# Performance work log

Measured on AMD Instinct MI355X. Metric: run time of the kernel, lower is better.

The kernel has to match this reference:

```python
import jax, jax.numpy as jnp
import numpy as np

B, T, S, E = 32, 256, 16, 400   # batch, max seq len, words per news, embed_size
H = 400                          # args.hidden_size (BiLSTM output width)
HC = H // 2                      # per-direction LSTM hidden
NH = 20                          # MHA heads (embed_size % 20 == 0)
DH = E // NH

def _p(k, shape, scale=0.05):
    return jax.random.normal(k, shape, dtype=jnp.float32) * scale

def setup_inputs():
    ks = jax.random.split(jax.random.key(0), 16)
    z = lambda n: jnp.zeros((n,), jnp.float32)
    return {
        "x1": jax.random.normal(ks[0], (B, T, E), dtype=jnp.float32),
        "x2": jax.random.normal(ks[1], (B, T, S, E), dtype=jnp.float32),
        "cate": jax.random.normal(ks[2], (B, T, 20), dtype=jnp.float32),
        "seq_lens": jnp.sort(jax.random.randint(ks[3], (B,), T // 2, T + 1))[::-1],
        "w_ih_f": _p(ks[4], (4 * HC, E)), "w_hh_f": _p(ks[5], (4 * HC, HC)),
        "b_ih_f": z(4 * HC), "b_hh_f": z(4 * HC),
        "w_ih_b": _p(ks[6], (4 * HC, E)), "w_hh_b": _p(ks[7], (4 * HC, HC)),
        "b_ih_b": z(4 * HC), "b_hh_b": z(4 * HC),
        "w_q": _p(ks[8], (E, E)), "b_q": z(E),
        "w_k": _p(ks[9], (E, E)), "b_k": z(E),
        "w_mlp_mha": _p(ks[10], (H, E)), "b_mlp_mha": z(H),
        "W_attn": _p(ks[11], (2 * H, 1)), "b_attn": z(1),
        "w_mlp": _p(ks[12], (E, 2 * H)), "b_mlp": z(E),
    }

def _lstm(x_tbe, w_ih, w_hh, b_ih, b_hh):
    # x_tbe: [T, B, in] -> [T, B, HC]; PyTorch gate order i,f,g,o
    h0 = jnp.zeros((x_tbe.shape[1], w_hh.shape[1]), x_tbe.dtype)
    def step(carry, xt):
        h, c = carry
        g = xt @ w_ih.T + h @ w_hh.T + (b_ih + b_hh)
        i, f, gg, o = jnp.split(g, 4, axis=-1)
        c = jax.nn.sigmoid(f) * c + jax.nn.sigmoid(i) * jnp.tanh(gg)
        h = jax.nn.sigmoid(o) * jnp.tanh(c)
        return (h, c), h
    _, hs = jax.lax.scan(step, (h0, h0), x_tbe)
    return hs

def reference(x1, x2, cate, seq_lens, w_ih_f, w_hh_f, b_ih_f, b_hh_f,
              w_ih_b, w_hh_b, b_ih_b, b_hh_b, w_q, b_q, w_k, b_k,
              w_mlp_mha, b_mlp_mha, W_attn, b_attn, w_mlp, b_mlp):
    t_idx = jnp.arange(T)
    valid = t_idx[None, :] < seq_lens[:, None]             # [B,T] ragged mask

    # --- per-news word self-attention pooling (only MHA attn weights used) ---
    tok = x2.reshape(B * T, S, E)
    q = (tok @ w_q.T + b_q).reshape(-1, S, NH, DH)
    k = (tok @ w_k.T + b_k).reshape(-1, S, NH, DH)
    scores = jnp.einsum('nqhd,nkhd->nhqk', q, k) * (1.0 / DH ** 0.5)
    w = jax.nn.softmax(scores, axis=-1).mean(axis=1)       # head-averaged [N,S,S]
    w = jax.nn.softmax(w.mean(axis=2), axis=1)             # [N,S]
    pooled = jnp.einsum('ns,nse->ne', w, tok)              # [N,E]
    x2p = (pooled @ w_mlp_mha.T + b_mlp_mha).reshape(B, T, H)

    # --- BiLSTM, equivalent to packed-sequence processing (per-length reversal) ---
    h_fwd = _lstm(x1.transpose(1, 0, 2), w_ih_f, w_hh_f, b_ih_f, b_hh_f).transpose(1, 0, 2)
    rev = jnp.clip(seq_lens[:, None] - 1 - t_idx[None, :], 0, T - 1)   # involution per seq
    x1r = jnp.take_along_axis(x1, rev[:, :, None], axis=1)
    h_bwd_r = _lstm(x1r.transpose(1, 0, 2), w_ih_b, w_hh_b, b_ih_b, b_hh_b).transpose(1, 0, 2)
    h_bwd = jnp.take_along_axis(h_bwd_r, rev[:, :, None], axis=1)
    h = jnp.concatenate([h_fwd, h_bwd], axis=-1)           # [B,T,H]

    # --- growing-window (causal) attention: score[b,t,s] = [h_s; x2p_t]@W_attn + b ---
    a = (h @ W_attn[:H]).squeeze(-1)                       # key term   [B,T]
    c = (x2p @ W_attn[H:]).squeeze(-1) + b_attn[0]         # query term [B,T]
    logits = a[:, None, :] + c[:, :, None]                 # [B,Tq,Tk]
    causal = t_idx[:, None] >= t_idx[None, :]
    attn = jax.nn.softmax(jnp.where(causal[None], logits, -1e30), axis=-1)
    x1_att = jnp.einsum('bts,bsh->bth', attn, h)           # [B,T,H]
    out = jnp.concatenate([x1_att, x2p], axis=-1) @ w_mlp.T + b_mlp
    return out * valid[:, :, None]                         # zeros beyond seq_lens
```

## Files before the change

kernel.cpp:

```cpp
#include <hip/hip_runtime.h>
#include <hip/hip_bf16.h>
#include <cstdint>
#include <cstddef>

typedef unsigned short u16;
typedef __attribute__((ext_vector_type(8))) short short8v;
typedef __attribute__((ext_vector_type(4))) short short4v;
typedef __attribute__((ext_vector_type(4))) float f32x4;
typedef __attribute__((ext_vector_type(4))) int i32x4;

#define MFMA16 __builtin_amdgcn_mfma_f32_16x16x32_bf16
#define MFMAI8 __builtin_amdgcn_mfma_i32_16x16x64_i8

__device__ __forceinline__ float bf2f(u16 u){
  union { unsigned int i; float f; } v; v.i = ((unsigned int)u) << 16; return v.f;
}
__device__ __forceinline__ u16 f2bf(float f){
  union { float f; unsigned int u; } v; v.f = f;
  unsigned int r = v.u + 0x7FFFu + ((v.u >> 16) & 1u);
  return (u16)(r >> 16);
}
__device__ __forceinline__ short8v szero(){
  short8v z;
  #pragma unroll
  for (int i = 0; i < 8; i++) z[i] = 0;
  return z;
}
__device__ __forceinline__ float sigm(float x){ return 1.0f/(1.0f + __expf(-x)); }
__device__ __forceinline__ float tanh_u(float x){
  float e = __expf(2.f*x);
  return 1.f - 2.f/(e + 1.f);
}
__device__ __forceinline__ void lds_barrier(){
  asm volatile("s_waitcnt lgkmcnt(0)" ::: "memory");
  __builtin_amdgcn_s_barrier();
  __builtin_amdgcn_sched_barrier(0);
}

__global__ void k0_cvt(const float* __restrict__ wq, const float* __restrict__ wk,
                       const float* __restrict__ wihf, const float* __restrict__ wihb,
                       const float* __restrict__ bihf, const float* __restrict__ bhhf,
                       const float* __restrict__ bihb, const float* __restrict__ bhhb,
                       u16* __restrict__ wqb, u16* __restrict__ wkb,
                       u16* __restrict__ wihfb, u16* __restrict__ wihbb,
                       float* __restrict__ bgf, float* __restrict__ bgb){
  int i = blockIdx.x*256 + threadIdx.x;
  if (i < 160000){ wqb[i] = f2bf(wq[i]); wkb[i] = f2bf(wk[i]); }
  if (i < 320000){ wihfb[i] = f2bf(wihf[i]); wihbb[i] = f2bf(wihb[i]); }
  if (i < 800){ bgf[i] = bihf[i] + bhhf[i]; bgb[i] = bihb[i] + bhhb[i]; }
}

__global__ void k0b_quant(const float* __restrict__ whhf, const float* __restrict__ whhb,
                          signed char* __restrict__ w8f, signed char* __restrict__ w8b,
                          float* __restrict__ sclf, float* __restrict__ sclb){
  const int tid = threadIdx.x, lane = tid & 63, wv = tid >> 6;
  const int widx = blockIdx.x*4 + wv;
  if (widx < 1600){
    int dir = widx / 800, g = widx - dir*800;
    const float* src = (dir ? whhb : whhf) + (size_t)g*200;
    float mx = 0.f;
    for (int j = lane; j < 200; j += 64) mx = fmaxf(mx, fabsf(src[j]));
    #pragma unroll
    for (int m = 32; m > 0; m >>= 1) mx = fmaxf(mx, __shfl_xor(mx, m, 64));
    float inv = (mx > 0.f) ? 127.f/mx : 0.f;
    int gt = g / 200, hl = g - gt*200;
    signed char* dst = (dir ? w8b : w8f) + (size_t)(gt*208 + hl)*256;
    int e0 = lane*4;
    unsigned int pack = 0u;
    if (e0 < 200){
      #pragma unroll
      for (int r = 0; r < 4; r++){
        int qv = __float2int_rn(src[e0+r]*inv);
        pack |= ((unsigned int)(qv & 255)) << (8*r);
      }
    }
    ((unsigned int*)dst)[lane] = pack;
    if (lane == 0) (dir ? sclb : sclf)[g] = mx / 16129.f;
  } else {
    int pr = widx - 1600;
    int dir = pr >> 5, rem = pr & 31, gt = rem >> 3, hl = 200 + (rem & 7);
    signed char* dst = (dir ? w8b : w8f) + (size_t)(gt*208 + hl)*256;
    ((unsigned int*)dst)[lane] = 0u;
  }
}

__launch_bounds__(512)
__global__ void k3_xw(const float* __restrict__ x1, const int* __restrict__ seq,
                      const u16* __restrict__ wihfb, const u16* __restrict__ wihbb,
                      const float* __restrict__ bgf, const float* __restrict__ bgb,
                      u16* __restrict__ xWf, u16* __restrict__ xWb){
  __shared__ u16 xf[12800];
  __shared__ u16 xb[12800];
  const int tid = threadIdx.x;
  const int t = blockIdx.x;
  for (int i = tid; i < 3200; i += 512){
    int b = i / 100, e4 = i - b*100;
    f32x4 vf = *(const f32x4*)&x1[((size_t)b*256 + t)*400 + e4*4];
    int rb = seq[b] - 1 - t; if (rb < 0) rb = 0;
    f32x4 vb = *(const f32x4*)&x1[((size_t)b*256 + rb)*400 + e4*4];
    short4v sf, sb;
    #pragma unroll
    for (int r = 0; r < 4; r++){ sf[r] = f2bf(vf[r]); sb[r] = f2bf(vb[r]); }
    ((short4v*)xf)[i] = sf;
    ((short4v*)xb)[i] = sb;
  }
  __syncthreads();
  const int lane = tid & 63, wv = tid >> 6;
  const int dir = wv >> 2, wl = wv & 3;
  const u16* xs = dir ? xb : xf;
  const u16* W  = dir ? wihbb : wihfb;
  const float* bg = dir ? bgb : bgf;
  u16* xW = dir ? xWb : xWf;
  const int q = lane & 15, kg = lane >> 4;
  short8v A[2][13];
  #pragma unroll
  for (int mt = 0; mt < 2; mt++)
    #pragma unroll
    for (int ksi = 0; ksi < 13; ksi++){
      int e0 = ksi*32 + kg*8;
      A[mt][ksi] = (e0 < 400) ? *(const short8v*)&xs[(mt*16 + q)*400 + e0] : szero();
    }
  for (int nt = wl; nt < 50; nt += 4){
    int g = nt*16 + q;
    float bv = bg[g];
    f32x4 acc0, acc1;
    acc0[0]=bv; acc0[1]=bv; acc0[2]=bv; acc0[3]=bv; acc1 = acc0;
    const u16* wrow = W + (size_t)g*400;
    #pragma unroll
    for (int ksi = 0; ksi < 13; ksi++){
      int e0 = ksi*32 + kg*8;
      short8v bf = (e0 < 400) ? *(const short8v*)&wrow[e0] : szero();
      acc0 = MFMA16(A[0][ksi], bf, acc0, 0,0,0);
      acc1 = MFMA16(A[1][ksi], bf, acc1, 0,0,0);
    }
    int gt = g / 200, hu = g - gt*200;
    #pragma unroll
    for (int r = 0; r < 4; r++){
      int bl = kg*4 + r;
      xW[(((size_t)t*32 +      bl)*200 + hu)*4 + gt] = f2bf(acc0[r]);
      xW[(((size_t)t*32 + 16 + bl)*200 + hu)*4 + gt] = f2bf(acc1[r]);
    }
  }
}

__device__ __forceinline__ void store_gate_f32(int p, const i32x4& acc, int q, int kg,
                                               float* gates, const float* scl_s){
  int gt = p/13, nt = p - gt*13;
  int hu0 = nt*16 + kg*4;
  if (hu0 < 200 && q < 4){
    const f32x4 s4 = *(const f32x4*)&scl_s[gt*200 + hu0];
    #pragma unroll
    for (int r = 0; r < 4; r++)
      gates[q*804 + (hu0+r)*4 + gt] = (float)acc[r]*s4[r];
  }
}

__launch_bounds__(512)
__global__ void k41_fused(const u16* __restrict__ xWf, const u16* __restrict__ xWb,
                          const signed char* __restrict__ w8f, const signed char* __restrict__ w8b,
                          const float* __restrict__ sclf, const float* __restrict__ sclb,
                          const int* __restrict__ seq, float* __restrict__ h_ws,
                          const float* __restrict__ x2,
                          const u16* __restrict__ wqb, const float* __restrict__ bq,
                          const u16* __restrict__ wkb, const float* __restrict__ bk,
                          float* __restrict__ pooled){
  __shared__ __align__(16) char smem[159232];
  const int tid = threadIdx.x;
  const int bid = blockIdx.x;

  if (bid < 16){
    __builtin_amdgcn_s_setprio(2);
    const int lane = tid & 63, wv = tid >> 6;
    const int q = lane & 15, kg = lane >> 4;
    signed char* h8   = (signed char*)smem;
    float* gates      = (float*)(smem + 4608);
    i32x4* pool       = (i32x4*)(smem + 17472);
    float* scl_s      = (float*)(smem + 33856);
    int* Ls           = (int*)(smem + 37056);
    const int dir = bid >> 3, grp = bid & 7;
    const u16* xWd = dir ? xWb : xWf;
    const signed char* w8 = dir ? w8b : w8f;
    const float* scl = dir ? sclb : sclf;
    if (tid < 4) Ls[tid] = seq[grp*4 + tid];
    for (int i = tid; i < 1152; i += 512) ((int*)h8)[i] = 0;
    for (int i = tid; i < 800; i += 512) scl_s[i] = scl[i];
    for (int idx = tid; idx < 1024; idx += 512){
      int s = idx >> 8, rem = idx & 255;
      int ksi = rem >> 6, l = rem & 63;
      int qq = l & 15, kk = l >> 4;
      pool[idx] = *(const i32x4*)&w8[(size_t)(3*208 + (9+s)*16 + qq)*256 + ksi*64 + kk*16];
    }
    i32x4 Wr[6][4];
    #pragma unroll
    for (int j = 0; j < 6; j++){
      int p = wv + 8*j, gt = p/13, nt = p - gt*13;
      #pragma unroll
      for (int ksi = 0; ksi < 4; ksi++)
        Wr[j][ksi] = *(const i32x4*)&w8[(size_t)(gt*208 + nt*16 + q)*256 + ksi*64 + kg*16];
    }
    float cst0 = 0.f, cst1 = 0.f;
    const int c0 = tid,        b0c = c0/200, hu0c = c0 - b0c*200;
    const int qd1 = tid + 512;
    const int b1c = qd1/200,   hu1c = qd1 - b1c*200;
    const int xoff0 = ((grp*4 + b0c)*200 + hu0c)*4;
    const int xoff1 = ((grp*4 + b1c)*200 + hu1c)*4;
    short4v xc0 = *(const short4v*)&xWd[xoff0];
    short4v xc1 = {0,0,0,0};
    if (tid < 288) xc1 = *(const short4v*)&xWd[xoff1];
    __syncthreads();
    #pragma unroll 1
    for (int t = 0; t < 256; t++){
      int tn = (t + 1 < 256) ? t + 1 : 255;
      const u16* xwn = xWd + (size_t)tn*25600;
      short4v xn0 = *(const short4v*)&xwn[xoff0];
      short4v xn1 = {0,0,0,0};
      if (tid < 288) xn1 = *(const short4v*)&xwn[xoff1];
      i32x4 bh[4];
      #pragma unroll
      for (int ksi = 0; ksi < 4; ksi++)
        bh[ksi] = *(const i32x4*)&h8[q*288 + ksi*64 + kg*16];
      #pragma unroll
      for (int j = 0; j < 6; j++){
        i32x4 acc = {0,0,0,0};
        #pragma unroll
        for (int ksi = 0; ksi < 4; ksi++)
          acc = MFMAI8(Wr[j][ksi], bh[ksi], acc, 0,0,0);
        store_gate_f32(wv + 8*j, acc, q, kg, gates, scl_s);
      }
      if (wv < 4){
        i32x4 acc = {0,0,0,0};
        #pragma unroll
        for (int ksi = 0; ksi < 4; ksi++)
          acc = MFMAI8(pool[(wv*4 + ksi)*64 + lane], bh[ksi], acc, 0,0,0);
        store_gate_f32(48 + wv, acc, q, kg, gates, scl_s);
      }
      lds_barrier();
      {
        const f32x4 g4 = *(const f32x4*)&gates[b0c*804 + hu0c*4];
        float gi = g4[0] + bf2f((u16)xc0[0]);
        float gf = g4[1] + bf2f((u16)xc0[1]);
        float gg = g4[2] + bf2f((u16)xc0[2]);
        float go = g4[3] + bf2f((u16)xc0[3]);
        float c = sigm(gf)*cst0 + sigm(gi)*tanh_u(gg);
        cst0 = c;
        float hv = sigm(go)*tanh_u(c);
        h8[b0c*288 + hu0c] = (signed char)__float2int_rn(hv*127.f);
        int gb = grp*4 + b0c;
        if (dir == 0){
          h_ws[((size_t)gb*256 + t)*400 + hu0c] = hv;
        } else {
          int tp = Ls[b0c] - 1 - t;
          if (tp >= 0) h_ws[((size_t)gb*256 + tp)*400 + 200 + hu0c] = hv;
        }
      }
      if (tid < 288){
        const f32x4 g4 = *(const f32x4*)&gates[b1c*804 + hu1c*4];
        float gi = g4[0] + bf2f((u16)xc1[0]);
        float gf = g4[1] + bf2f((u16)xc1[1]);
        float gg = g4[2] + bf2f((u16)xc1[2]);
        float go = g4[3] + bf2f((u16)xc1[3]);
        float c = sigm(gf)*cst1 + sigm(gi)*tanh_u(gg);
        cst1 = c;
        float hv = sigm(go)*tanh_u(c);
        h8[b1c*288 + hu1c] = (signed char)__float2int_rn(hv*127.f);
        int gb = grp*4 + b1c;
        if (dir == 0){
          h_ws[((size_t)gb*256 + t)*400 + hu1c] = hv;
        } else {
          int tp = Ls[b1c] - 1 - t;
          if (tp >= 0) h_ws[((size_t)gb*256 + tp)*400 + 200 + hu1c] = hv;
        }
      }
      lds_barrier();
      xc0 = xn0; xc1 = xn1;
    }
  } else {
    const int htid = tid & 255;
    const int hf   = tid >> 8;
    char* hs = smem + hf*79616;
    u16* tok0  = (u16*)hs;
    u16* qsb   = (u16*)(hs + 25600);
    u16* ksb   = (u16*)(hs + 51456);
    float* msum= (float*)(hs + 77312);
    float* tval= (float*)(hs + 79360);
    float* attw= (float*)(hs + 79488);
    const int lane = htid & 63, wv = htid >> 6;
    const int q = lane & 15, kg = lane >> 4;
    const int kb = bid - 16;
    const size_t n0 = (size_t)kb*4 + hf*2;
    const float* src = x2 + n0*6400;
    for (int i = htid; i < 512; i += 256) ((float*)msum)[i] = 0.f;
    for (int i = htid; i < 3200; i += 256){
      f32x4 v = *(const f32x4*)&src[(size_t)i*4];
      short4v s; s[0]=f2bf(v[0]); s[1]=f2bf(v[1]); s[2]=f2bf(v[2]); s[3]=f2bf(v[3]);
      int j = i / 1600, r = i - j*1600;
      ((short4v*)(tok0 + j*6400))[r] = s;
    }
    __syncthreads();
    {
      const int proj = wv >> 1;
      const int ntbase = (wv & 1) ? 13 : 0;
      const int ntcnt  = (wv & 1) ? 12 : 13;
      const u16* W    = proj ? wkb : wqb;
      const float* bias = proj ? bk : bq;
      short8v A[2][13];
      #pragma unroll
      for (int j = 0; j < 2; j++)
        #pragma unroll
        for (int ksi = 0; ksi < 13; ksi++){
          int e0 = ksi*32 + kg*8;
          A[j][ksi] = (e0 < 400) ? *(const short8v*)&tok0[j*6400 + q*400 + e0] : szero();
        }
      u16* d0 = (proj ? ksb : qsb);
      u16* d1 = d0 + 6464;
      for (int ti = 0; ti < ntcnt; ti++){
        int col = (ntbase + ti)*16 + q;
        float bv = bias[col];
        f32x4 acc0, acc1;
        acc0[0]=bv; acc0[1]=bv; acc0[2]=bv; acc0[3]=bv; acc1 = acc0;
        const u16* wrow = W + (size_t)col*400;
        #pragma unroll
        for (int ksi = 0; ksi < 13; ksi++){
          int e0 = ksi*32 + kg*8;
          short8v bf = (e0 < 400) ? *(const short8v*)&wrow[e0] : szero();
          acc0 = MFMA16(A[0][ksi], bf, acc0, 0, 0, 0);
          acc1 = MFMA16(A[1][ksi], bf, acc1, 0, 0, 0);
        }
        #pragma unroll
        for (int r = 0; r < 4; r++){
          d0[(kg*4+r)*404 + col] = f2bf(acc0[r]);
          d1[(kg*4+r)*404 + col] = f2bf(acc1[r]);
        }
      }
    }
    __syncthreads();
    for (int rr = 0; rr < 3; rr++){
      int row = htid + rr*256;
      if (row < 640){
        int j = row / 320, r2 = row - j*320;
        int hh = r2 >> 4, sq = r2 & 15;
        const u16* qrow = qsb + j*6464 + sq*404 + hh*20;
        float qv[20];
        #pragma unroll
        for (int d5 = 0; d5 < 5; d5++){
          short4v v = *(const short4v*)&qrow[d5*4];
          qv[d5*4+0]=bf2f((u16)v[0]); qv[d5*4+1]=bf2f((u16)v[1]);
          qv[d5*4+2]=bf2f((u16)v[2]); qv[d5*4+3]=bf2f((u16)v[3]);
        }
        float sc[16]; float mx = -1e30f;
        const u16* kbase = ksb + j*6464 + hh*20;
        #pragma unroll
        for (int sk = 0; sk < 16; sk++){
          const u16* krow = kbase + sk*404;
          float s = 0.f;
          #pragma unroll
          for (int d5 = 0; d5 < 5; d5++){
            short4v v = *(const short4v*)&krow[d5*4];
            s += qv[d5*4+0]*bf2f((u16)v[0]) + qv[d5*4+1]*bf2f((u16)v[1])
               + qv[d5*4+2]*bf2f((u16)v[2]) + qv[d5*4+3]*bf2f((u16)v[3]);
          }
          s *= 0.22360679775f;
          sc[sk] = s; mx = fmaxf(mx, s);
        }
        float sum = 0.f;
        #pragma unroll
        for (int sk = 0; sk < 16; sk++){ sc[sk] = __expf(sc[sk]-mx); sum += sc[sk]; }
        float inv = 0.05f/sum;
        #pragma unroll
        for (int sk = 0; sk < 16; sk++){
          float v = sc[sk]*inv;
          v += __shfl_xor(v, 16, 64);
          v += __shfl_xor(v, 32, 64);
          if (kg == 0) atomicAdd(&msum[j*256 + sq*16 + sk], v);
        }
      }
    }
    __syncthreads();
    if (htid < 32){
      int j = htid >> 4, sq = htid & 15;
      float s = 0.f;
      #pragma unroll
      for (int sk = 0; sk < 16; sk++) s += msum[j*256 + sq*16+sk];
      tval[j*16 + sq] = s * 0.0625f;
    }
    __syncthreads();
    if (htid < 2){
      float mx = -1e30f;
      for (int i = 0; i < 16; i++) mx = fmaxf(mx, tval[htid*16+i]);
      float sum = 0.f; float ev[16];
      for (int i = 0; i < 16; i++){ ev[i] = __expf(tval[htid*16+i]-mx); sum += ev[i]; }
      float inv = 1.f/sum;
      for (int i = 0; i < 16; i++) attw[htid*16+i] = ev[i]*inv;
    }
    __syncthreads();
    for (int e = htid; e < 800; e += 256){
      int j = e / 400, c = e - j*400;
      float acc = 0.f;
      #pragma unroll
      for (int s = 0; s < 16; s++) acc += attw[j*16+s]*bf2f(tok0[j*6400 + s*400 + c]);
      pooled[(n0+j)*400 + c] = acc;
    }
  }
}

__global__ void k2_x2p(const float* __restrict__ pooled, const float* __restrict__ wmha,
                       const float* __restrict__ bmha, float* __restrict__ x2p){
  __shared__ float rows[3200];
  const int tid = threadIdx.x;
  const size_t n0 = (size_t)blockIdx.x*8;
  for (int i = tid; i < 3200; i += 256) rows[i] = pooled[n0*400 + i];
  __syncthreads();
  for (int j = tid; j < 400; j += 256){
    float bv = bmha[j];
    float acc[8];
    #pragma unroll
    for (int r = 0; r < 8; r++) acc[r] = bv;
    const float* wr = wmha + (size_t)j*400;
    for (int e = 0; e < 400; e += 4){
      const f32x4 w4 = *(const f32x4*)&wr[e];
      #pragma unroll
      for (int r = 0; r < 8; r++){
        const f32x4 x4 = *(const f32x4*)&rows[r*400 + e];
        acc[r] += x4[0]*w4[0] + x4[1]*w4[1] + x4[2]*w4[2] + x4[3]*w4[3];
      }
    }
    #pragma unroll
    for (int r = 0; r < 8; r++) x2p[(n0+r)*400 + j] = acc[r];
  }
}

__global__ void k4b_fill(const int* __restrict__ seq, float* __restrict__ h_ws,
                         const float* __restrict__ wattn,
                         float* __restrict__ a_ws, float* __restrict__ amax_ws){
  __shared__ float a_lds[256];
  const int b = blockIdx.x;
  const int tid = threadIdx.x;
  const int lane = tid & 63, wv = tid >> 6;
  const int L = seq[b];
  const int cnt = (256 - L)*200;
  const float* srcf = h_ws + ((size_t)b*256 + (L-1))*400 + 200;
  for (int i = tid; i < cnt; i += 256){
    int tt = L + i/200, cc = i - (i/200)*200;
    h_ws[((size_t)b*256 + tt)*400 + 200 + cc] = srcf[cc];
  }
  __syncthreads();
  for (int row = wv*64; row < wv*64 + 64; row++){
    float s = 0.f;
    for (int j = lane; j < 400; j += 64)
      s += h_ws[((size_t)b*256 + row)*400 + j] * wattn[j];
    #pragma unroll
    for (int m = 32; m > 0; m >>= 1) s += __shfl_xor(s, m, 64);
    if (lane == 0) a_lds[row] = s;
  }
  __syncthreads();
  a_ws[b*256 + tid] = a_lds[tid];
  if (tid < 64){
    float m = fmaxf(fmaxf(a_lds[tid], a_lds[tid+64]), fmaxf(a_lds[tid+128], a_lds[tid+192]));
    #pragma unroll
    for (int mm = 32; mm > 0; mm >>= 1) m = fmaxf(m, __shfl_xor(m, mm, 64));
    if (tid == 0) amax_ws[b] = m;
  }
}

__launch_bounds__(256)
__global__ void k5_attn(const float* __restrict__ h_ws, const float* __restrict__ a_ws,
                        const float* __restrict__ amax_ws, float* __restrict__ x1_att){
  __shared__ float tile[256*52];
  __shared__ float wl[256];
  const int tid = threadIdx.x;
  const int b = blockIdx.x >> 3, ch = blockIdx.x & 7;
  const int c0 = ch*50;
  wl[tid] = __expf(a_ws[b*256 + tid] - amax_ws[b]);
  for (int i = tid; i < 12800; i += 256){
    int r = i / 50, c = i - r*50;
    tile[r*52 + c] = h_ws[((size_t)b*256 + r)*400 + c0 + c];
  }
  __syncthreads();
  if (tid < 50){
    float den = 0.f, num = 0.f;
    #pragma unroll 4
    for (int t = 0; t < 256; t++){
      float w = wl[t];
      den += w;
      num += w * tile[t*52 + tid];
      tile[t*52 + tid] = num/den;
    }
  }
  __syncthreads();
  for (int i = tid; i < 12800; i += 256){
    int r = i / 50, c = i - r*50;
    x1_att[((size_t)b*256 + r)*400 + c0 + c] = tile[r*52 + c];
  }
}

__global__ void k6_out(const float* __restrict__ x1_att, const float* __restrict__ x2p,
                       const float* __restrict__ wmlp, const float* __restrict__ bmlp,
                       const int* __restrict__ seq, float* __restrict__ out){
  __shared__ float rows[8*800];
  const int tid = threadIdx.x;
  const size_t n0 = (size_t)blockIdx.x*8;
  const int b = (int)(n0 >> 8), t0 = (int)(n0 & 255);
  const int L = seq[b];
  for (int i = tid; i < 3200; i += 256){
    int r = i / 400, e = i - r*400;
    rows[r*800 + e]       = x1_att[(n0 + r)*400 + e];
    rows[r*800 + 400 + e] = x2p  [(n0 + r)*400 + e];
  }
  __syncthreads();
  for (int e = tid; e < 400; e += 256){
    float bv = bmlp[e];
    float acc[8];
    #pragma unroll
    for (int r = 0; r < 8; r++) acc[r] = bv;
    const float* wr = wmlp + (size_t)e*800;
    for (int j = 0; j < 800; j += 4){
      const f32x4 w4 = *(const f32x4*)&wr[j];
      #pragma unroll
      for (int r = 0; r < 8; r++){
        const f32x4 x4 = *(const f32x4*)&rows[r*800 + j];
        acc[r] += x4[0]*w4[0] + x4[1]*w4[1] + x4[2]*w4[2] + x4[3]*w4[3];
      }
    }
    #pragma unroll
    for (int r = 0; r < 8; r++){
      float v = (t0 + r < L) ? acc[r] : 0.f;
      out[(n0 + r)*400 + e] = v;
    }
  }
}

extern "C" void kernel_launch(void* const* d_in, const int* in_sizes, int n_in,
                              void* d_out, int out_size, void* d_ws, size_t ws_size,
                              hipStream_t stream){
  const float* x1   = (const float*)d_in[0];
  const float* x2   = (const float*)d_in[1];
  const int*   seq  = (const int*)d_in[3];
  const float* wihf = (const float*)d_in[4];
  const float* whhf = (const float*)d_in[5];
  const float* bihf = (const float*)d_in[6];
  const float* bhhf = (const float*)d_in[7];
  const float* wihb = (const float*)d_in[8];
  const float* whhb = (const float*)d_in[9];
  const float* bihb = (const float*)d_in[10];
  const float* bhhb = (const float*)d_in[11];
  const float* wq   = (const float*)d_in[12];
  const float* bq   = (const float*)d_in[13];
  const float* wk   = (const float*)d_in[14];
  const float* bk   = (const float*)d_in[15];
  const float* wmha = (const float*)d_in[16];
  const float* bmha = (const float*)d_in[17];
  const float* wattn= (const float*)d_in[18];
  const float* wmlp = (const float*)d_in[20];
  const float* bmlp = (const float*)d_in[21];
  float* out = (float*)d_out;

  char* ws = (char*)d_ws;
  u16*  wqb    = (u16*)(ws + 0);
  u16*  wkb    = (u16*)(ws + 320000);
  u16*  wihfb  = (u16*)(ws + 640000);
  u16*  wihbb  = (u16*)(ws + 1280000);
  signed char* w8f  = (signed char*)(ws + 1920000);
  signed char* w8b  = (signed char*)(ws + 2132992);
  float* sclf  = (float*)(ws + 2345984);
  float* sclb  = (float*)(ws + 2349184);
  float* bgf   = (float*)(ws + 2352384);
  float* bgb   = (float*)(ws + 2355584);
  float* pooled= (float*)(ws + 2359296);
  float* x2p   = (float*)(ws + 15466496);
  u16*  xWf    = (u16*)(ws + 28573696);
  u16*  xWb    = (u16*)(ws + 41680896);
  float* h_ws  = (float*)(ws + 54788096);
  float* a_ws  = (float*)(ws + 67895296);
  float* amax_ws=(float*)(ws + 67928064);
  float* x1_att= (float*)(ws + 28573696);

  k0_cvt  <<<dim3(1250), dim3(256), 0, stream>>>(wq, wk, wihf, wihb,
                                                 bihf, bhhf, bihb, bhhb,
                                                 wqb, wkb, wihfb, wihbb, bgf, bgb);
  k0b_quant<<<dim3(416), dim3(256), 0, stream>>>(whhf, whhb, w8f, w8b, sclf, sclb);
  k3_xw   <<<dim3(256),  dim3(512), 0, stream>>>(x1, seq, wihfb, wihbb, bgf, bgb, xWf, xWb);
  k41_fused<<<dim3(2064), dim3(512), 0, stream>>>(xWf, xWb, w8f, w8b, sclf, sclb, seq, h_ws,
                                                  x2, wqb, bq, wkb, bk, pooled);
  k2_x2p  <<<dim3(1024), dim3(256), 0, stream>>>(pooled, wmha, bmha, x2p);
  k4b_fill<<<dim3(32),   dim3(256), 0, stream>>>(seq, h_ws, wattn, a_ws, amax_ws);
  k5_attn <<<dim3(256),  dim3(256), 0, stream>>>(h_ws, a_ws, amax_ws, x1_att);
  k6_out  <<<dim3(1024), dim3(256), 0, stream>>>(x1_att, x2p, wmlp, bmlp, seq, out);
}
```

Measured before the change: 956.2 us.

## Rewrite final MLP projection with bf16 MFMA and larger row tiles

The output projection kernel now converts the concatenated activations to bf16 in shared memory and computes the 800->400 projection with 16x16x32 bf16 MFMA instructions. The weight matrix is pre-converted to bf16 in the existing conversion kernel. Each block now handles 32 rows with 512 threads instead of 8 rows, which increases weight reuse. This replaces scalar fp32 FMA loops, at the cost of bf16 rounding error in the final layer.

```diff
diff --git a/kernel.cpp b/kernel.cpp
--- a/kernel.cpp
+++ b/kernel.cpp
@@ -39,14 +39,16 @@
 
 __global__ void k0_cvt(const float* __restrict__ wq, const float* __restrict__ wk,
                        const float* __restrict__ wihf, const float* __restrict__ wihb,
+                       const float* __restrict__ wmlp,
                        const float* __restrict__ bihf, const float* __restrict__ bhhf,
                        const float* __restrict__ bihb, const float* __restrict__ bhhb,
                        u16* __restrict__ wqb, u16* __restrict__ wkb,
                        u16* __restrict__ wihfb, u16* __restrict__ wihbb,
+                       u16* __restrict__ wmlpb,
                        float* __restrict__ bgf, float* __restrict__ bgb){
   int i = blockIdx.x*256 + threadIdx.x;
   if (i < 160000){ wqb[i] = f2bf(wq[i]); wkb[i] = f2bf(wk[i]); }
-  if (i < 320000){ wihfb[i] = f2bf(wihf[i]); wihbb[i] = f2bf(wihb[i]); }
+  if (i < 320000){ wihfb[i] = f2bf(wihf[i]); wihbb[i] = f2bf(wihb[i]); wmlpb[i] = f2bf(wmlp[i]); }
   if (i < 800){ bgf[i] = bihf[i] + bhhf[i]; bgb[i] = bihb[i] + bhhb[i]; }
 }
 
@@ -493,38 +495,53 @@
   }
 }
 
+__launch_bounds__(512)
 __global__ void k6_out(const float* __restrict__ x1_att, const float* __restrict__ x2p,
-                       const float* __restrict__ wmlp, const float* __restrict__ bmlp,
+                       const u16* __restrict__ wmlpb, const float* __restrict__ bmlp,
                        const int* __restrict__ seq, float* __restrict__ out){
-  __shared__ float rows[8*800];
+  __shared__ __align__(16) u16 rows[32*800];
   const int tid = threadIdx.x;
-  const size_t n0 = (size_t)blockIdx.x*8;
+  const size_t n0 = (size_t)blockIdx.x*32;
   const int b = (int)(n0 >> 8), t0 = (int)(n0 & 255);
   const int L = seq[b];
-  for (int i = tid; i < 3200; i += 256){
-    int r = i / 400, e = i - r*400;
-    rows[r*800 + e]       = x1_att[(n0 + r)*400 + e];
-    rows[r*800 + 400 + e] = x2p  [(n0 + r)*400 + e];
+  for (int c = tid; c < 6400; c += 512){
+    int r = c / 200, u = c - r*200;
+    const float* sp = (u < 100) ? &x1_att[(n0 + r)*400 + u*4]
+                                : &x2p  [(n0 + r)*400 + (u-100)*4];
+    f32x4 v = *(const f32x4*)sp;
+    int cb = (u < 100) ? u*4 : 400 + (u-100)*4;
+    short4v s;
+    #pragma unroll
+    for (int r2 = 0; r2 < 4; r2++) s[r2] = f2bf(v[r2]);
+    *(short4v*)&rows[r*800 + cb] = s;
   }
   __syncthreads();
-  for (int e = tid; e < 400; e += 256){
-    float bv = bmlp[e];
-    float acc[8];
-    #pragma unroll
-    for (int r = 0; r < 8; r++) acc[r] = bv;
-    const float* wr = wmlp + (size_t)e*800;
-    for (int j = 0; j < 800; j += 4){
-      const f32x4 w4 = *(const f32x4*)&wr[j];
-      #pragma unroll
-      for (int r = 0; r < 8; r++){
-        const f32x4 x4 = *(const f32x4*)&rows[r*800 + j];
-        acc[r] += x4[0]*w4[0] + x4[1]*w4[1] + x4[2]*w4[2] + x4[3]*w4[3];
-      }
-    }
-    #pragma unroll
-    for (int r = 0; r < 8; r++){
-      float v = (t0 + r < L) ? acc[r] : 0.f;
-      out[(n0 + r)*400 + e] = v;
+  const int lane = tid & 63, wv = tid >> 6;
+  const int q = lane & 15, kg = lane >> 4;
+  const int ntasks = (wv == 0) ? 4 : 3;
+  for (int ti = 0; ti < ntasks; ti++){
+    int nt = (ti < 3) ? (wv + ti*8) : 24;
+    int col = nt*16 + q;
+    float bv = bmlp[col];
+    f32x4 acc0, acc1;
+    acc0[0]=bv; acc0[1]=bv; acc0[2]=bv; acc0[3]=bv; acc1 = acc0;
+    const u16* wrow = wmlpb + (size_t)col*800;
+    #pragma unroll
+    for (int ksi = 0; ksi < 25; ksi++){
+      int e0 = ksi*32 + kg*8;
+      short8v bf = *(const short8v*)&wrow[e0];
+      short8v a0 = *(const short8v*)&rows[q*800 + e0];
+      short8v a1 = *(const short8v*)&rows[(16+q)*800 + e0];
+      acc0 = MFMA16(a0, bf, acc0, 0,0,0);
+      acc1 = MFMA16(a1, bf, acc1, 0,0,0);
+    }
+    #pragma unroll
+    for (int r = 0; r < 4; r++){
+      int rl = kg*4 + r;
+      float v0 = (t0 + rl      < L) ? acc0[r] : 0.f;
+      float v1 = (t0 + 16 + rl < L) ? acc1[r] : 0.f;
+      out[(n0 +      rl)*400 + col] = v0;
+      out[(n0 + 16 + rl)*400 + col] = v1;
     }
   }
 }
@@ -572,11 +589,12 @@
   float* h_ws  = (float*)(ws + 54788096);
   float* a_ws  = (float*)(ws + 67895296);
   float* amax_ws=(float*)(ws + 67928064);
+  u16*  wmlpb  = (u16*)(ws + 67928192);
   float* x1_att= (float*)(ws + 28573696);
 
-  k0_cvt  <<<dim3(1250), dim3(256), 0, stream>>>(wq, wk, wihf, wihb,
+  k0_cvt  <<<dim3(1250), dim3(256), 0, stream>>>(wq, wk, wihf, wihb, wmlp,
                                                  bihf, bhhf, bihb, bhhb,
-                                                 wqb, wkb, wihfb, wihbb, bgf, bgb);
+                                                 wqb, wkb, wihfb, wihbb, wmlpb, bgf, bgb);
   k0b_quant<<<dim3(416), dim3(256), 0, stream>>>(whhf, whhb, w8f, w8b, sclf, sclb);
   k3_xw   <<<dim3(256),  dim3(512), 0, stream>>>(x1, seq, wihfb, wihbb, bgf, bgb, xWf, xWb);
   k41_fused<<<dim3(2064), dim3(512), 0, stream>>>(xWf, xWb, w8f, w8b, sclf, sclb, seq, h_ws,
@@ -584,5 +602,5 @@
   k2_x2p  <<<dim3(1024), dim3(256), 0, stream>>>(pooled, wmha, bmha, x2p);
   k4b_fill<<<dim3(32),   dim3(256), 0, stream>>>(seq, h_ws, wattn, a_ws, amax_ws);
   k5_attn <<<dim3(256),  dim3(256), 0, stream>>>(h_ws, a_ws, amax_ws, x1_att);
-  k6_out  <<<dim3(1024), dim3(256), 0, stream>>>(x1_att, x2p, wmlp, bmlp, seq, out);
-}
+  k6_out  <<<dim3(256),  dim3(512), 0, stream>>>(x1_att, x2p, wmlpb, bmlp, seq, out);
+}
```

After: 818.0 us. 14.5% less time.
